# Performance work log

Hardware: AMD Instinct MI355X
Metric: run time of the kernel (lower is better)

Reference implementation:

```python
import jax, jax.numpy as jnp
import numpy as np

N_NODES = 50000

def gcn_conv(x, src, dst, W, b, n_nodes):
    # PyG GCNConv: add self-loops, symmetric normalization D^-1/2 (A+I) D^-1/2, then bias
    loop = jnp.arange(n_nodes)
    s = jnp.concatenate([src, loop])
    d = jnp.concatenate([dst, loop])
    deg = jax.ops.segment_sum(jnp.ones(s.shape[0], x.dtype), d, num_segments=n_nodes)
    dinv = jnp.where(deg > 0, jax.lax.rsqrt(deg), 0.0)
    norm = dinv[s] * dinv[d]                      # [E+N]
    h = x @ W                                      # [N, out]
    msg = h[s] * norm[:, None]                     # gather + scale
    out = jax.ops.segment_sum(msg, d, num_segments=n_nodes)  # scatter-add
    return out + b

def setup_inputs() -> dict:
    key = jax.random.key(0)
    ks = jax.random.split(key, 8)
    x = jax.random.normal(ks[0], (N_NODES, 128), jnp.float32)
    edge_index = jax.random.randint(ks[1], (2, 800000), 0, N_NODES)
    def glorot(k, fan_in, fan_out):
        lim = np.sqrt(6.0 / (fan_in + fan_out)).astype(np.float32)
        return jax.random.uniform(k, (fan_in, fan_out), jnp.float32, -lim, lim)
    return {
        "x": x,
        "edge_index": edge_index,
        "conv_w1": glorot(ks[2], 128, 64), "conv_b1": jnp.zeros((64,), jnp.float32),
        "conv_w2": glorot(ks[3], 64, 64),  "conv_b2": jnp.zeros((64,), jnp.float32),
        "fc_w1": glorot(ks[4], 64, 32),    "fc_b1": jnp.zeros((32,), jnp.float32),
        "fc_w2": glorot(ks[5], 32, 1),     "fc_b2": jnp.zeros((1,), jnp.float32),
    }

def reference(x, edge_index, conv_w1, conv_b1, conv_w2, conv_b2, fc_w1, fc_b1, fc_w2, fc_b2):
    src, dst = edge_index[0], edge_index[1]
    h = jnp.tanh(gcn_conv(x, src, dst, conv_w1, conv_b1, N_NODES))
    h = jnp.tanh(gcn_conv(h, src, dst, conv_w2, conv_b2, N_NODES))
    h = jnp.tanh(h @ fc_w1 + fc_b1)  # dropout is identity at inference
    return h @ fc_w2 + fc_b2          # [N, 1]
```

## Files before the change

### kernel.cpp

```cpp
#include <hip/hip_runtime.h>
#include <math.h>

#define TPB 256
#define NBK_MAX 512
#define CAP 4096
#define FILL_CAP 4096
#define SC_CH 16

typedef short bf16x8 __attribute__((ext_vector_type(8)));
typedef float f32x4 __attribute__((ext_vector_type(4)));

__device__ __forceinline__ unsigned short rne_bf16(float f) {
  unsigned u = __float_as_uint(f);
  return (unsigned short)((u + 0x7fffu + ((u >> 16) & 1u)) >> 16);
}
__device__ __forceinline__ float bf16_f(unsigned short v) {
  return __uint_as_float((unsigned)v << 16);
}
__device__ __forceinline__ float rl_f(float v, int l) {
  return __int_as_float(__builtin_amdgcn_readlane(__float_as_int(v), l));
}
__device__ __forceinline__ float ftanh(float x) {
  float xc = fminf(fmaxf(x, -15.f), 15.f);
  float e = __expf(2.f * xc);
  return (e - 1.f) * __builtin_amdgcn_rcpf(e + 1.f);
}

__global__ __launch_bounds__(TPB) void k_init(int* __restrict__ gcur,
                                              unsigned short* __restrict__ h1z,
                                              unsigned short* __restrict__ h2z,
                                              int NBK, int N) {
  int i = blockIdx.x * TPB + threadIdx.x;
  if (i < NBK) gcur[i] = i * CAP;
  if (blockIdx.x == 0) {
    if (threadIdx.x < 32)
      ((unsigned*)(h1z + ((size_t)N << 6)))[threadIdx.x] = 0;
    else if (threadIdx.x < 64)
      ((unsigned*)(h2z + ((size_t)N << 6)))[threadIdx.x - 32] = 0;
  }
}

__global__ __launch_bounds__(TPB) void k_bscatter(const int* __restrict__ src,
                                                  const int* __restrict__ dst,
                                                  int* __restrict__ gcur,
                                                  unsigned* __restrict__ e2,
                                                  int E, int NBK) {
  __shared__ int h[NBK_MAX];
  __shared__ int base[NBK_MAX];
  int tid = threadIdx.x, blk = blockIdx.x, G = gridDim.x;
  int chunk = (E + G - 1) / G, lo = blk * chunk, hi = min(E, lo + chunk);
  for (int t0 = lo; t0 < hi; t0 += TPB * SC_CH) {
    int sv[SC_CH], dv[SC_CH];
    for (int b = tid; b < NBK; b += TPB) h[b] = 0;
    __syncthreads();
#pragma unroll
    for (int u = 0; u < SC_CH; ++u) {
      int e = t0 + u * TPB + tid;
      if (e < hi) {
        dv[u] = dst[e];
        sv[u] = src[e];
        atomicAdd(&h[dv[u] >> 7], 1);
      } else {
        dv[u] = -1;
      }
    }
    __syncthreads();
    for (int b = tid; b < NBK; b += TPB) {
      int c = h[b];
      if (c) {
        int o = atomicAdd(&gcur[b], c);
        base[b] = min(o, (b + 1) * CAP - c);
      }
    }
    __syncthreads();
    for (int b = tid; b < NBK; b += TPB) h[b] = 0;
    __syncthreads();
#pragma unroll
    for (int u = 0; u < SC_CH; ++u) {
      if (dv[u] >= 0) {
        int bk = dv[u] >> 7;
        int r = atomicAdd(&h[bk], 1);
        e2[base[bk] + r] = ((unsigned)sv[u] << 7) | (unsigned)(dv[u] & 127);
      }
    }
    __syncthreads();
  }
}

__global__ __launch_bounds__(TPB) void k_build(const unsigned* __restrict__ e2,
                                               const int* __restrict__ gcur,
                                               int* __restrict__ rowptr,
                                               int* __restrict__ rowend,
                                               float* __restrict__ dinv,
                                               int* __restrict__ col, int N) {
  __shared__ int c[128], sc[128], cur[128];
  __shared__ int buf[FILL_CAP];
  int tid = threadIdx.x, b = blockIdx.x;
  int st = b * CAP;
  int en = min(gcur[b], st + FILL_CAP);
  int len = en - st;
  if (tid < 128) c[tid] = 0;
  __syncthreads();
  for (int i = st + tid; i < en; i += TPB) atomicAdd(&c[e2[i] & 127u], 1);
  __syncthreads();
  if (tid < 128) sc[tid] = c[tid];
  __syncthreads();
  for (int o = 1; o < 128; o <<= 1) {
    int v = (tid >= o && tid < 128) ? sc[tid - o] : 0;
    __syncthreads();
    if (tid < 128) sc[tid] += v;
    __syncthreads();
  }
  if (tid < 128) {
    int excl = sc[tid] - c[tid];
    cur[tid] = excl;
    int node = b * 128 + tid;
    if (node < N) {
      rowptr[node] = st + excl;
      rowend[node] = st + excl + c[tid];
      dinv[node] = rsqrtf((float)(c[tid] + 1));
    }
  }
  __syncthreads();
  for (int i = st + tid; i < en; i += TPB) {
    unsigned v = e2[i];
    int p = atomicAdd(&cur[v & 127u], 1);
    buf[p] = (int)(v >> 7);
  }
  __syncthreads();
  for (int i = tid; i < len; i += TPB) col[st + i] = buf[i];
}

template <int K>
__global__ __launch_bounds__(TPB) void k_mm(const float* __restrict__ Ap,
                                            const float* __restrict__ W,
                                            const float* __restrict__ dinv,
                                            unsigned short* __restrict__ Hout, int N) {
  constexpr int P = K + 8;
  __shared__ unsigned short sHi[64 * P];
  __shared__ unsigned short sLo[64 * P];
  int tid = threadIdx.x;
  for (int i = tid; i < K * 64; i += TPB) {
    int k = i >> 6, n = i & 63;
    float w = W[i];
    unsigned short hb = rne_bf16(w);
    sHi[n * P + k] = hb;
    sLo[n * P + k] = rne_bf16(w - bf16_f(hb));
  }
  __syncthreads();
  int wave = tid >> 6, lane = tid & 63;
  int oct = lane >> 4, l15 = lane & 15;
  int base = blockIdx.x * 64 + wave * 16;
  int arow = base + l15;
  if (arow >= N) arow = N - 1;
  f32x4 acc[4] = {};
#pragma unroll
  for (int s = 0; s < K / 32; ++s) {
    bf16x8 ahi, alo;
    const float* ap = Ap + (size_t)arow * K + s * 32 + oct * 8;
    float4 f0 = *(const float4*)ap;
    float4 f1 = *(const float4*)(ap + 4);
    float fv[8] = {f0.x, f0.y, f0.z, f0.w, f1.x, f1.y, f1.z, f1.w};
#pragma unroll
    for (int j = 0; j < 8; ++j) {
      unsigned short hb = rne_bf16(fv[j]);
      ahi[j] = (short)hb;
      alo[j] = (short)rne_bf16(fv[j] - bf16_f(hb));
    }
#pragma unroll
    for (int t = 0; t < 4; ++t) {
      bf16x8 bh = *(const bf16x8*)(sHi + (t * 16 + l15) * P + s * 32 + oct * 8);
      bf16x8 bl = *(const bf16x8*)(sLo + (t * 16 + l15) * P + s * 32 + oct * 8);
      acc[t] = __builtin_amdgcn_mfma_f32_16x16x32_bf16(ahi, bh, acc[t], 0, 0, 0);
      acc[t] = __builtin_amdgcn_mfma_f32_16x16x32_bf16(ahi, bl, acc[t], 0, 0, 0);
      acc[t] = __builtin_amdgcn_mfma_f32_16x16x32_bf16(alo, bh, acc[t], 0, 0, 0);
    }
  }
#pragma unroll
  for (int r = 0; r < 4; ++r) {
    int row = base + oct * 4 + r;
    if (row < N) {
      float dv = dinv[row];
#pragma unroll
      for (int t = 0; t < 4; ++t)
        Hout[(size_t)row * 64 + t * 16 + l15] = rne_bf16(acc[t][r] * dv);
    }
  }
}

__device__ __forceinline__ void agg_pair(int i0, int i1,
                                         const unsigned short* __restrict__ H,
                                         const int* __restrict__ rowptr,
                                         const int* __restrict__ rowend,
                                         const int* __restrict__ col, int NS,
                                         float& o0, float& o1) {
  int lane = threadIdx.x & 63;
  float a0 = bf16_f(H[((size_t)i0 << 6) + lane]);
  float a1 = bf16_f(H[((size_t)i1 << 6) + lane]);
  int b0 = rowptr[i0], e0 = rowend[i0];
  int b1 = rowptr[i1], e1 = rowend[i1];
  int jj0 = b0 + lane, jj1 = b1 + lane;
  int sv0 = col[(jj0 < e0) ? jj0 : b0];
  if (jj0 >= e0) sv0 = NS;
  int sv1 = col[(jj1 < e1) ? jj1 : b1];
  if (jj1 >= e1) sv1 = NS;
  int l0 = e0 - b0, l1 = e1 - b1;
  int lm = max(l0, l1);
  if (lm > 64) lm = 64;
  for (int t = 0; t < lm; t += 8) {
    int s0 = __builtin_amdgcn_readlane(sv0, t + 0);
    int s1 = __builtin_amdgcn_readlane(sv0, t + 1);
    int s2 = __builtin_amdgcn_readlane(sv0, t + 2);
    int s3 = __builtin_amdgcn_readlane(sv0, t + 3);
    int s4 = __builtin_amdgcn_readlane(sv0, t + 4);
    int s5 = __builtin_amdgcn_readlane(sv0, t + 5);
    int s6 = __builtin_amdgcn_readlane(sv0, t + 6);
    int s7 = __builtin_amdgcn_readlane(sv0, t + 7);
    int u0 = __builtin_amdgcn_readlane(sv1, t + 0);
    int u1 = __builtin_amdgcn_readlane(sv1, t + 1);
    int u2 = __builtin_amdgcn_readlane(sv1, t + 2);
    int u3 = __builtin_amdgcn_readlane(sv1, t + 3);
    int u4 = __builtin_amdgcn_readlane(sv1, t + 4);
    int u5 = __builtin_amdgcn_readlane(sv1, t + 5);
    int u6 = __builtin_amdgcn_readlane(sv1, t + 6);
    int u7 = __builtin_amdgcn_readlane(sv1, t + 7);
    unsigned short g0 = H[((size_t)s0 << 6) + lane];
    unsigned short g1 = H[((size_t)s1 << 6) + lane];
    unsigned short g2 = H[((size_t)s2 << 6) + lane];
    unsigned short g3 = H[((size_t)s3 << 6) + lane];
    unsigned short g4 = H[((size_t)s4 << 6) + lane];
    unsigned short g5 = H[((size_t)s5 << 6) + lane];
    unsigned short g6 = H[((size_t)s6 << 6) + lane];
    unsigned short g7 = H[((size_t)s7 << 6) + lane];
    unsigned short q0 = H[((size_t)u0 << 6) + lane];
    unsigned short q1 = H[((size_t)u1 << 6) + lane];
    unsigned short q2 = H[((size_t)u2 << 6) + lane];
    unsigned short q3 = H[((size_t)u3 << 6) + lane];
    unsigned short q4 = H[((size_t)u4 << 6) + lane];
    unsigned short q5 = H[((size_t)u5 << 6) + lane];
    unsigned short q6 = H[((size_t)u6 << 6) + lane];
    unsigned short q7 = H[((size_t)u7 << 6) + lane];
    a0 += bf16_f(g0); a0 += bf16_f(g1); a0 += bf16_f(g2); a0 += bf16_f(g3);
    a0 += bf16_f(g4); a0 += bf16_f(g5); a0 += bf16_f(g6); a0 += bf16_f(g7);
    a1 += bf16_f(q0); a1 += bf16_f(q1); a1 += bf16_f(q2); a1 += bf16_f(q3);
    a1 += bf16_f(q4); a1 += bf16_f(q5); a1 += bf16_f(q6); a1 += bf16_f(q7);
  }
  for (int c0 = b0 + 64; c0 < e0; c0 += 64) {
    int jj = c0 + lane;
    int sv = col[(jj < e0) ? jj : b0];
    if (jj >= e0) sv = NS;
    int lim = min(64, e0 - c0);
    for (int t = 0; t < lim; ++t) {
      int s = __builtin_amdgcn_readlane(sv, t);
      a0 += bf16_f(H[((size_t)s << 6) + lane]);
    }
  }
  for (int c0 = b1 + 64; c0 < e1; c0 += 64) {
    int jj = c0 + lane;
    int sv = col[(jj < e1) ? jj : b1];
    if (jj >= e1) sv = NS;
    int lim = min(64, e1 - c0);
    for (int t = 0; t < lim; ++t) {
      int s = __builtin_amdgcn_readlane(sv, t);
      a1 += bf16_f(H[((size_t)s << 6) + lane]);
    }
  }
  o0 = a0;
  o1 = a1;
}

__global__ __launch_bounds__(TPB, 4) void k_aggmm(const unsigned short* __restrict__ H1,
                                                  const int* __restrict__ rowptr,
                                                  const int* __restrict__ rowend,
                                                  const int* __restrict__ col,
                                                  const float* __restrict__ dinv,
                                                  const float* __restrict__ bias,
                                                  const float* __restrict__ W2,
                                                  unsigned short* __restrict__ H2, int N) {
  __shared__ float w2s[64 * 64];
  int tid = threadIdx.x;
  for (int i = tid; i < 64 * 64; i += TPB) w2s[i] = W2[i];
  __syncthreads();
  int lane = tid & 63, wid = tid >> 6;
  float w2r[64];
#pragma unroll
  for (int k = 0; k < 64; ++k) w2r[k] = w2s[k * 64 + lane];
  float bfeat = bias[lane];
  int gw = gridDim.x * 4;
  int npairs = (N + 1) / 2;
  for (int p = blockIdx.x * 4 + wid; p < npairs; p += gw) {
    int i0 = 2 * p;
    int i1 = min(2 * p + 1, N - 1);
    float v0, v1;
    agg_pair(i0, i1, H1, rowptr, rowend, col, N, v0, v1);
    float t0 = ftanh(dinv[i0] * v0 + bfeat);
    float t1 = ftanh(dinv[i1] * v1 + bfeat);
    float m0 = 0.f, m1 = 0.f;
#pragma unroll
    for (int k = 0; k < 64; ++k) {
      m0 += rl_f(t0, k) * w2r[k];
      m1 += rl_f(t1, k) * w2r[k];
    }
    H2[((size_t)i0 << 6) + lane] = rne_bf16(m0 * dinv[i0]);
    if (i1 != i0)
      H2[((size_t)i1 << 6) + lane] = rne_bf16(m1 * dinv[i1]);
  }
}

__global__ __launch_bounds__(TPB) void k_aggfc(const unsigned short* __restrict__ H2,
                                               const int* __restrict__ rowptr,
                                               const int* __restrict__ rowend,
                                               const int* __restrict__ col,
                                               const float* __restrict__ dinv,
                                               const float* __restrict__ bias,
                                               const float* __restrict__ fw1,
                                               const float* __restrict__ fb1,
                                               const float* __restrict__ fw2,
                                               const float* __restrict__ fb2,
                                               float* __restrict__ fout, int N) {
  __shared__ float sw1t[32 * 66];
  __shared__ float sb1[32];
  __shared__ float sw2[32];
  __shared__ float sA[8 * 64];
  int tid = threadIdx.x;
  for (int i = tid; i < 32 * 64; i += TPB) {
    int j = i >> 6, k = i & 63;
    sw1t[j * 66 + k] = fw1[k * 32 + j];
  }
  if (tid < 32) { sb1[tid] = fb1[tid]; sw2[tid] = fw2[tid]; }
  __syncthreads();
  int wid = tid >> 6, lane = tid & 63;
  float bfeat = bias[lane];
  float b2v = fb2[0];
  int ngroups = (N + 7) / 8;
  for (int grp = blockIdx.x; grp < ngroups; grp += gridDim.x) {
    int base = grp * 8;
    int i0 = min(base + wid * 2, N - 1);
    int i1 = min(base + wid * 2 + 1, N - 1);
    float v0, v1;
    agg_pair(i0, i1, H2, rowptr, rowend, col, N, v0, v1);
    sA[(wid * 2 + 0) * 64 + lane] = ftanh(dinv[i0] * v0 + bfeat);
    sA[(wid * 2 + 1) * 64 + lane] = ftanh(dinv[i1] * v1 + bfeat);
    __syncthreads();
    {
      int n = tid >> 5, j = tid & 31;
      int node = base + n;
      if (node < N) {
        float acc = sb1[j];
        const float2* ar = (const float2*)(sA + n * 64);
        const float2* wr = (const float2*)(sw1t + j * 66);
#pragma unroll
        for (int k2 = 0; k2 < 32; ++k2) {
          float2 av = ar[k2];
          float2 wv = wr[k2];
          acc += av.x * wv.x + av.y * wv.y;
        }
        float t = ftanh(acc) * sw2[j];
#pragma unroll
        for (int o = 1; o < 32; o <<= 1) t += __shfl_xor(t, o);
        if (j == 0) fout[node] = t + b2v;
      }
    }
    __syncthreads();
  }
}


extern "C" void kernel_launch(void* const* d_in, const int* in_sizes, int n_in,
                              void* d_out, int out_size, void* d_ws, size_t ws_size,
                              hipStream_t stream) {
  const float* x   = (const float*)d_in[0];
  const int*   ei  = (const int*)d_in[1];
  const float* w1  = (const float*)d_in[2];
  const float* b1  = (const float*)d_in[3];
  const float* w2  = (const float*)d_in[4];
  const float* b2  = (const float*)d_in[5];
  const float* fw1 = (const float*)d_in[6];
  const float* fb1 = (const float*)d_in[7];
  const float* fw2 = (const float*)d_in[8];
  const float* fb2 = (const float*)d_in[9];
  float* out = (float*)d_out;

  int N = in_sizes[0] / 128;
  int E = in_sizes[1] / 2;
  const int* src = ei;
  const int* dst = ei + E;

  const int G   = 256;
  const int NBK = (N + 127) / 128;

  char* p = (char*)d_ws;
  size_t off = 0;
  auto take = [&](size_t bytes) -> void* {
    void* r = p + off;
    off += (bytes + 255) & ~(size_t)255;
    return r;
  };
  int*            gcur   = (int*)take((size_t)NBK * 4);
  int*            rowptr = (int*)take((size_t)N * 4);
  int*            rowend = (int*)take((size_t)N * 4);
  float*          dinv   = (float*)take((size_t)N * 4);
  unsigned*       e2     = (unsigned*)take((size_t)NBK * CAP * 4);
  int*            col    = (int*)take(((size_t)NBK * CAP + 64) * 4);
  unsigned short* h1     = (unsigned short*)take((size_t)(N + 1) * 64 * 2);
  unsigned short* h2     = (unsigned short*)take((size_t)(N + 1) * 64 * 2);
  (void)ws_size; (void)n_in; (void)out_size;

  k_init<<<(NBK + TPB - 1) / TPB, TPB, 0, stream>>>(gcur, h1, h2, NBK, N);
  k_bscatter<<<G, TPB, 0, stream>>>(src, dst, gcur, e2, E, NBK);
  k_build<<<NBK, TPB, 0, stream>>>(e2, gcur, rowptr, rowend, dinv, col, N);

  int gmm = (N + 63) / 64;
  k_mm<128><<<gmm, TPB, 0, stream>>>(x, w1, dinv, h1, N);
  k_aggmm<<<2048, TPB, 0, stream>>>(h1, rowptr, rowend, col, dinv, b1, w2, h2, N);
  k_aggfc<<<3125, TPB, 0, stream>>>(h2, rowptr, rowend, col, dinv, b2,
                                    fw1, fb1, fw2, fb2, out, N);
}
```

Baseline: 194.4 us.

## Aggregate one node per wave with 16-wide gathers, batch 32 nodes per FC block

The paired two-node aggregation is replaced with a single-node routine. It issues 16 independent row gathers per step instead of 8 per node. k_aggmm now processes one node per wave iteration. k_aggfc now has each wave aggregate 8 nodes into a 32-node shared tile before running the FC stage over four passes, and both grids shrink to 1024 blocks. This trades the cross-node memory-level parallelism of the pair scheme for deeper per-node gather batching and fewer block barriers, at the cost of wasted padded gathers for short rows and a larger shared tile.

```diff
diff --git a/kernel.cpp b/kernel.cpp
--- a/kernel.cpp
+++ b/kernel.cpp
@@ -188,85 +188,39 @@
   }
 }
 
-__device__ __forceinline__ void agg_pair(int i0, int i1,
-                                         const unsigned short* __restrict__ H,
+__device__ __forceinline__ float agg_one(int i, const unsigned short* __restrict__ H,
                                          const int* __restrict__ rowptr,
                                          const int* __restrict__ rowend,
-                                         const int* __restrict__ col, int NS,
-                                         float& o0, float& o1) {
+                                         const int* __restrict__ col, int NS) {
   int lane = threadIdx.x & 63;
-  float a0 = bf16_f(H[((size_t)i0 << 6) + lane]);
-  float a1 = bf16_f(H[((size_t)i1 << 6) + lane]);
-  int b0 = rowptr[i0], e0 = rowend[i0];
-  int b1 = rowptr[i1], e1 = rowend[i1];
-  int jj0 = b0 + lane, jj1 = b1 + lane;
-  int sv0 = col[(jj0 < e0) ? jj0 : b0];
-  if (jj0 >= e0) sv0 = NS;
-  int sv1 = col[(jj1 < e1) ? jj1 : b1];
-  if (jj1 >= e1) sv1 = NS;
-  int l0 = e0 - b0, l1 = e1 - b1;
-  int lm = max(l0, l1);
-  if (lm > 64) lm = 64;
-  for (int t = 0; t < lm; t += 8) {
-    int s0 = __builtin_amdgcn_readlane(sv0, t + 0);
-    int s1 = __builtin_amdgcn_readlane(sv0, t + 1);
-    int s2 = __builtin_amdgcn_readlane(sv0, t + 2);
-    int s3 = __builtin_amdgcn_readlane(sv0, t + 3);
-    int s4 = __builtin_amdgcn_readlane(sv0, t + 4);
-    int s5 = __builtin_amdgcn_readlane(sv0, t + 5);
-    int s6 = __builtin_amdgcn_readlane(sv0, t + 6);
-    int s7 = __builtin_amdgcn_readlane(sv0, t + 7);
-    int u0 = __builtin_amdgcn_readlane(sv1, t + 0);
-    int u1 = __builtin_amdgcn_readlane(sv1, t + 1);
-    int u2 = __builtin_amdgcn_readlane(sv1, t + 2);
-    int u3 = __builtin_amdgcn_readlane(sv1, t + 3);
-    int u4 = __builtin_amdgcn_readlane(sv1, t + 4);
-    int u5 = __builtin_amdgcn_readlane(sv1, t + 5);
-    int u6 = __builtin_amdgcn_readlane(sv1, t + 6);
-    int u7 = __builtin_amdgcn_readlane(sv1, t + 7);
-    unsigned short g0 = H[((size_t)s0 << 6) + lane];
-    unsigned short g1 = H[((size_t)s1 << 6) + lane];
-    unsigned short g2 = H[((size_t)s2 << 6) + lane];
-    unsigned short g3 = H[((size_t)s3 << 6) + lane];
-    unsigned short g4 = H[((size_t)s4 << 6) + lane];
-    unsigned short g5 = H[((size_t)s5 << 6) + lane];
-    unsigned short g6 = H[((size_t)s6 << 6) + lane];
-    unsigned short g7 = H[((size_t)s7 << 6) + lane];
-    unsigned short q0 = H[((size_t)u0 << 6) + lane];
-    unsigned short q1 = H[((size_t)u1 << 6) + lane];
-    unsigned short q2 = H[((size_t)u2 << 6) + lane];
-    unsigned short q3 = H[((size_t)u3 << 6) + lane];
-    unsigned short q4 = H[((size_t)u4 << 6) + lane];
-    unsigned short q5 = H[((size_t)u5 << 6) + lane];
-    unsigned short q6 = H[((size_t)u6 << 6) + lane];
-    unsigned short q7 = H[((size_t)u7 << 6) + lane];
-    a0 += bf16_f(g0); a0 += bf16_f(g1); a0 += bf16_f(g2); a0 += bf16_f(g3);
-    a0 += bf16_f(g4); a0 += bf16_f(g5); a0 += bf16_f(g6); a0 += bf16_f(g7);
-    a1 += bf16_f(q0); a1 += bf16_f(q1); a1 += bf16_f(q2); a1 += bf16_f(q3);
-    a1 += bf16_f(q4); a1 += bf16_f(q5); a1 += bf16_f(q6); a1 += bf16_f(q7);
-  }
-  for (int c0 = b0 + 64; c0 < e0; c0 += 64) {
-    int jj = c0 + lane;
-    int sv = col[(jj < e0) ? jj : b0];
-    if (jj >= e0) sv = NS;
-    int lim = min(64, e0 - c0);
-    for (int t = 0; t < lim; ++t) {
-      int s = __builtin_amdgcn_readlane(sv, t);
-      a0 += bf16_f(H[((size_t)s << 6) + lane]);
-    }
-  }
-  for (int c0 = b1 + 64; c0 < e1; c0 += 64) {
-    int jj = c0 + lane;
-    int sv = col[(jj < e1) ? jj : b1];
-    if (jj >= e1) sv = NS;
-    int lim = min(64, e1 - c0);
-    for (int t = 0; t < lim; ++t) {
-      int s = __builtin_amdgcn_readlane(sv, t);
-      a1 += bf16_f(H[((size_t)s << 6) + lane]);
-    }
-  }
-  o0 = a0;
-  o1 = a1;
+  float acc = bf16_f(H[((size_t)i << 6) + lane]);
+  int beg = rowptr[i], end = rowend[i];
+  int jj = beg + lane;
+  int sv = col[(jj < end) ? jj : beg];
+  if (jj >= end) sv = NS;
+  int len = end - beg;
+  int lim = min(len, 64);
+  for (int t = 0; t < lim; t += 16) {
+    int s[16];
+#pragma unroll
+    for (int g = 0; g < 16; ++g) s[g] = __builtin_amdgcn_readlane(sv, t + g);
+    unsigned short hv[16];
+#pragma unroll
+    for (int g = 0; g < 16; ++g) hv[g] = H[((size_t)s[g] << 6) + lane];
+#pragma unroll
+    for (int g = 0; g < 16; ++g) acc += bf16_f(hv[g]);
+  }
+  for (int c0 = beg + 64; c0 < end; c0 += 64) {
+    int j2 = c0 + lane;
+    int s2 = col[(j2 < end) ? j2 : beg];
+    if (j2 >= end) s2 = NS;
+    int l2 = min(64, end - c0);
+    for (int t = 0; t < l2; ++t) {
+      int s = __builtin_amdgcn_readlane(s2, t);
+      acc += bf16_f(H[((size_t)s << 6) + lane]);
+    }
+  }
+  return acc;
 }
 
 __global__ __launch_bounds__(TPB, 4) void k_aggmm(const unsigned short* __restrict__ H1,
@@ -281,47 +235,39 @@
   int tid = threadIdx.x;
   for (int i = tid; i < 64 * 64; i += TPB) w2s[i] = W2[i];
   __syncthreads();
-  int lane = tid & 63, wid = tid >> 6;
+  int lane = tid & 63, wave = tid >> 6;
   float w2r[64];
 #pragma unroll
   for (int k = 0; k < 64; ++k) w2r[k] = w2s[k * 64 + lane];
   float bfeat = bias[lane];
+  int wid = blockIdx.x * 4 + wave;
   int gw = gridDim.x * 4;
-  int npairs = (N + 1) / 2;
-  for (int p = blockIdx.x * 4 + wid; p < npairs; p += gw) {
-    int i0 = 2 * p;
-    int i1 = min(2 * p + 1, N - 1);
-    float v0, v1;
-    agg_pair(i0, i1, H1, rowptr, rowend, col, N, v0, v1);
-    float t0 = ftanh(dinv[i0] * v0 + bfeat);
-    float t1 = ftanh(dinv[i1] * v1 + bfeat);
-    float m0 = 0.f, m1 = 0.f;
-#pragma unroll
-    for (int k = 0; k < 64; ++k) {
-      m0 += rl_f(t0, k) * w2r[k];
-      m1 += rl_f(t1, k) * w2r[k];
-    }
-    H2[((size_t)i0 << 6) + lane] = rne_bf16(m0 * dinv[i0]);
-    if (i1 != i0)
-      H2[((size_t)i1 << 6) + lane] = rne_bf16(m1 * dinv[i1]);
-  }
-}
-
-__global__ __launch_bounds__(TPB) void k_aggfc(const unsigned short* __restrict__ H2,
-                                               const int* __restrict__ rowptr,
-                                               const int* __restrict__ rowend,
-                                               const int* __restrict__ col,
-                                               const float* __restrict__ dinv,
-                                               const float* __restrict__ bias,
-                                               const float* __restrict__ fw1,
-                                               const float* __restrict__ fb1,
-                                               const float* __restrict__ fw2,
-                                               const float* __restrict__ fb2,
-                                               float* __restrict__ fout, int N) {
+  for (int i = wid; i < N; i += gw) {
+    float di = dinv[i];
+    float v = agg_one(i, H1, rowptr, rowend, col, N);
+    float t0 = ftanh(di * v + bfeat);
+    float m = 0.f;
+#pragma unroll
+    for (int k = 0; k < 64; ++k) m += rl_f(t0, k) * w2r[k];
+    H2[((size_t)i << 6) + lane] = rne_bf16(m * di);
+  }
+}
+
+__global__ __launch_bounds__(TPB, 4) void k_aggfc(const unsigned short* __restrict__ H2,
+                                                  const int* __restrict__ rowptr,
+                                                  const int* __restrict__ rowend,
+                                                  const int* __restrict__ col,
+                                                  const float* __restrict__ dinv,
+                                                  const float* __restrict__ bias,
+                                                  const float* __restrict__ fw1,
+                                                  const float* __restrict__ fb1,
+                                                  const float* __restrict__ fw2,
+                                                  const float* __restrict__ fb2,
+                                                  float* __restrict__ fout, int N) {
   __shared__ float sw1t[32 * 66];
   __shared__ float sb1[32];
   __shared__ float sw2[32];
-  __shared__ float sA[8 * 64];
+  __shared__ float sA[32 * 64];
   int tid = threadIdx.x;
   for (int i = tid; i < 32 * 64; i += TPB) {
     int j = i >> 6, k = i & 63;
@@ -329,21 +275,23 @@
   }
   if (tid < 32) { sb1[tid] = fb1[tid]; sw2[tid] = fw2[tid]; }
   __syncthreads();
-  int wid = tid >> 6, lane = tid & 63;
+  int wave = tid >> 6, lane = tid & 63;
   float bfeat = bias[lane];
   float b2v = fb2[0];
-  int ngroups = (N + 7) / 8;
+  int ngroups = (N + 31) / 32;
   for (int grp = blockIdx.x; grp < ngroups; grp += gridDim.x) {
-    int base = grp * 8;
-    int i0 = min(base + wid * 2, N - 1);
-    int i1 = min(base + wid * 2 + 1, N - 1);
-    float v0, v1;
-    agg_pair(i0, i1, H2, rowptr, rowend, col, N, v0, v1);
-    sA[(wid * 2 + 0) * 64 + lane] = ftanh(dinv[i0] * v0 + bfeat);
-    sA[(wid * 2 + 1) * 64 + lane] = ftanh(dinv[i1] * v1 + bfeat);
-    __syncthreads();
-    {
-      int n = tid >> 5, j = tid & 31;
+    int base = grp * 32;
+    for (int q = 0; q < 8; ++q) {
+      int n = wave * 8 + q;
+      int i = min(base + n, N - 1);
+      float v = agg_one(i, H2, rowptr, rowend, col, N);
+      sA[n * 64 + lane] = ftanh(dinv[i] * v + bfeat);
+    }
+    __syncthreads();
+    int nn = tid >> 5, j = tid & 31;
+#pragma unroll
+    for (int pass = 0; pass < 4; ++pass) {
+      int n = pass * 8 + nn;
       int node = base + n;
       if (node < N) {
         float acc = sb1[j];
@@ -412,7 +360,7 @@
 
   int gmm = (N + 63) / 64;
   k_mm<128><<<gmm, TPB, 0, stream>>>(x, w1, dinv, h1, N);
-  k_aggmm<<<2048, TPB, 0, stream>>>(h1, rowptr, rowend, col, dinv, b1, w2, h2, N);
-  k_aggfc<<<3125, TPB, 0, stream>>>(h2, rowptr, rowend, col, dinv, b2,
+  k_aggmm<<<1024, TPB, 0, stream>>>(h1, rowptr, rowend, col, dinv, b1, w2, h2, N);
+  k_aggfc<<<1024, TPB, 0, stream>>>(h2, rowptr, rowend, col, dinv, b2,
                                     fw1, fb1, fw2, fb2, out, N);
 }
```

Result: slower. 202.3 us (+4.1%).
